# Kernel optimization log

Measured on AMD Instinct MI355X. Metric: run time of the kernel, lower is better.

The kernel has to match this reference:

```python
import jax, jax.numpy as jnp
import numpy as np

N_HEADS = 16
D_HEAD = 64
D_MODEL = 1024


def apply_rotary_emb(t, cos, sin):
    # t: (B, H, T, D), cos/sin: (T, D//2) -> half-split rotation
    d2 = t.shape[-1] // 2
    t1, t2 = t[..., :d2], t[..., d2:]
    cos = cos[None, None, :, :]
    sin = sin[None, None, :, :]
    return jnp.concatenate([t1 * cos - t2 * sin, t1 * sin + t2 * cos], axis=-1)


def setup_inputs() -> dict:
    key = jax.random.key(0)
    ks = jax.random.split(key, 8)
    B, T = 2, 2048
    x = jax.random.normal(ks[0], (B, T, D_MODEL), dtype=jnp.float32)
    # rotary cache built from standard inv-freq schedule
    inv_freq = 1.0 / (10000.0 ** (jnp.arange(0, D_HEAD, 2, dtype=jnp.float32) / D_HEAD))
    ang = jnp.arange(T, dtype=jnp.float32)[:, None] * inv_freq[None, :]  # (T, D/2)
    cos, sin = jnp.cos(ang), jnp.sin(ang)
    s = 1.0 / np.sqrt(D_MODEL)
    W_q = jax.random.normal(ks[1], (D_MODEL, N_HEADS * D_HEAD), dtype=jnp.float32) * s
    W_k = jax.random.normal(ks[2], (D_MODEL, N_HEADS * D_HEAD), dtype=jnp.float32) * s
    W_v = jax.random.normal(ks[3], (D_MODEL, N_HEADS * D_HEAD), dtype=jnp.float32) * s
    W_out = jax.random.normal(ks[4], (N_HEADS * D_HEAD, D_MODEL), dtype=jnp.float32) * s
    return {"x": x, "cos": cos, "sin": sin, "W_q": W_q, "W_k": W_k, "W_v": W_v, "W_out": W_out}


def reference(x, cos, sin, W_q, W_k, W_v, W_out):
    B, T, _ = x.shape
    def split_heads(t):
        return t.reshape(B, T, N_HEADS, D_HEAD).transpose(0, 2, 1, 3)  # (B,H,T,D)
    q = split_heads(x @ W_q)
    k = split_heads(x @ W_k)
    v = split_heads(x @ W_v)
    q = apply_rotary_emb(q, cos, sin)
    k = apply_rotary_emb(k, cos, sin)
    scores = jnp.einsum('bhqd,bhkd->bhqk', q, k) / np.sqrt(D_HEAD).astype(np.float32)
    causal = jnp.triu(jnp.ones((T, T), dtype=bool), k=1)
    scores = jnp.where(causal[None, None], -jnp.inf, scores)
    attn = jax.nn.softmax(scores, axis=-1)
    z = jnp.einsum('bhqk,bhkd->bhqd', attn, v)
    z = z.transpose(0, 2, 1, 3).reshape(B, T, N_HEADS * D_HEAD)
    return z @ W_out
```

## Files before the change

### kernel.cpp

```cpp
#include <hip/hip_runtime.h>

typedef __attribute__((ext_vector_type(4))) float f32x4;
typedef __attribute__((ext_vector_type(8))) short short8;
typedef __attribute__((ext_vector_type(8))) unsigned short u16x8;
typedef __attribute__((ext_vector_type(4))) unsigned short u16x4;
typedef __attribute__((ext_vector_type(2))) unsigned int u32x2;

#define D_MODEL 1024
#define NHEADS 16
#define T_SEQ 2048
#define M_TOT 4096

__device__ __forceinline__ unsigned short f2bf(float f) {
    union { float f; unsigned int u; } v; v.f = f;
    return (unsigned short)((v.u + 0x7fffu + ((v.u >> 16) & 1u)) >> 16);
}
__device__ __forceinline__ float bf2f(unsigned short b) {
    union { unsigned int u; float f; } v; v.u = ((unsigned int)b) << 16;
    return v.f;
}
__device__ __forceinline__ float bcf(unsigned int u) {
    union { unsigned int u; float f; } v; v.u = u; return v.f;
}
__device__ __forceinline__ unsigned int cvtpk_bf16(float lo, float hi) {
    unsigned int r;
    asm("v_cvt_pk_bf16_f32 %0, %1, %2" : "=v"(r) : "v"(lo), "v"(hi));
    return r;
}

#define GLD0(dst, addr) \
    asm volatile("global_load_dwordx4 %0, %1, off" : "=v"(dst) : "v"(addr) : "memory")
#define WAITV0() do { asm volatile("s_waitcnt vmcnt(0)" ::: "memory"); \
                      __builtin_amdgcn_sched_barrier(0); } while (0)
#define LBAR() do { asm volatile("s_waitcnt lgkmcnt(0)" ::: "memory"); \
                    __builtin_amdgcn_s_barrier(); \
                    __builtin_amdgcn_sched_barrier(0); } while (0)

__global__ __launch_bounds__(256) void convert_x_kernel(const float* __restrict__ X,
                                                        unsigned short* __restrict__ Xb) {
    const int i = (blockIdx.x * 256 + threadIdx.x) * 4;
    const float4 v = *(const float4*)(X + i);
    u16x4 r;
    r.x = f2bf(v.x); r.y = f2bf(v.y); r.z = f2bf(v.z); r.w = f2bf(v.w);
    *(u16x4*)(Xb + i) = r;
}

__global__ __launch_bounds__(256) void transpose_w_kernel(const float* __restrict__ W0,
                                                          const float* __restrict__ W1,
                                                          const float* __restrict__ W2,
                                                          const float* __restrict__ W3,
                                                          unsigned short* __restrict__ Wt0) {
    __shared__ float tile[64][65];
    const int z = blockIdx.z;
    const float* W = (z == 0) ? W0 : (z == 1) ? W1 : (z == 2) ? W2 : W3;
    unsigned short* Wt = Wt0 + (size_t)z * D_MODEL * D_MODEL;
    const int n0 = blockIdx.x * 64, k0 = blockIdx.y * 64;
    for (int i = threadIdx.x; i < 4096; i += 256) {
        const int r = i >> 6, c = i & 63;
        tile[r][c] = W[(size_t)(k0 + r) * D_MODEL + n0 + c];
    }
    __syncthreads();
    for (int i = threadIdx.x; i < 4096; i += 256) {
        const int r = i >> 6, c = i & 63;
        Wt[(size_t)(n0 + r) * D_MODEL + k0 + c] = f2bf(tile[c][r]);
    }
}

#define TN_G 128
#define BK_G 32
#define BKP_G 36

template<int MI, int OUTMODE>
__global__ __launch_bounds__(256) void gemm_kernel(
    const unsigned short* __restrict__ A,
    const unsigned short* __restrict__ Bt0,
    void* __restrict__ Cout0,
    const float* __restrict__ cosp,
    const float* __restrict__ sinp)
{
    constexpr int TMc = MI * 32;
    constexpr int NA = (TMc * 4) / 256;
    __shared__ unsigned short sA[TMc * BKP_G];
    __shared__ unsigned short sB[TN_G * BKP_G];

    const int tid = threadIdx.x;
    const int wid = tid >> 6;
    const int lane = tid & 63;
    const int quad = lane >> 4;
    const int l16 = lane & 15;
    const int wm = wid >> 1, wn = wid & 1;
    const int m0 = blockIdx.x * TMc, n0 = blockIdx.y * TN_G;
    const int z = blockIdx.z;
    const unsigned short* Bt = Bt0 + (size_t)z * D_MODEL * D_MODEL;

    f32x4 acc[MI][4] = {};

    for (int k0 = 0; k0 < D_MODEL; k0 += BK_G) {
        u16x8 av[NA], bv[2];
        #pragma unroll
        for (int i = 0; i < NA; ++i) {
            const int c = tid + i * 256, r = c >> 2, sg = (c & 3) * 8;
            av[i] = *(const u16x8*)(A + (size_t)(m0 + r) * D_MODEL + k0 + sg);
        }
        #pragma unroll
        for (int i = 0; i < 2; ++i) {
            const int c = tid + i * 256, r = c >> 2, sg = (c & 3) * 8;
            bv[i] = *(const u16x8*)(Bt + (size_t)(n0 + r) * D_MODEL + k0 + sg);
        }
        __syncthreads();
        #pragma unroll
        for (int i = 0; i < NA; ++i) {
            const int c = tid + i * 256, r = c >> 2, sg = (c & 3) * 8;
            *(u16x8*)&sA[r * BKP_G + sg] = av[i];
        }
        #pragma unroll
        for (int i = 0; i < 2; ++i) {
            const int c = tid + i * 256, r = c >> 2, sg = (c & 3) * 8;
            *(u16x8*)&sB[r * BKP_G + sg] = bv[i];
        }
        __syncthreads();

        short8 af[MI], bf[4];
        #pragma unroll
        for (int i = 0; i < MI; ++i)
            af[i] = *(const short8*)&sA[(wm * (MI * 16) + i * 16 + l16) * BKP_G + quad * 8];
        #pragma unroll
        for (int i = 0; i < 4; ++i)
            bf[i] = *(const short8*)&sB[(wn * 64 + i * 16 + l16) * BKP_G + quad * 8];
        #pragma unroll
        for (int mi = 0; mi < MI; ++mi)
            #pragma unroll
            for (int ni = 0; ni < 4; ++ni)
                acc[mi][ni] = __builtin_amdgcn_mfma_f32_16x16x32_bf16(af[mi], bf[ni], acc[mi][ni], 0, 0, 0);
    }

    if constexpr (OUTMODE == 0) {
        float* C = (float*)Cout0;
        #pragma unroll
        for (int mi = 0; mi < MI; ++mi) {
            const int mb = m0 + wm * (MI * 16) + mi * 16 + quad * 4;
            #pragma unroll
            for (int ni = 0; ni < 4; ++ni) {
                const int n = n0 + wn * 64 + ni * 16 + l16;
                #pragma unroll
                for (int r = 0; r < 4; ++r)
                    C[(size_t)(mb + r) * D_MODEL + n] = acc[mi][ni][r];
            }
        }
    } else {
        unsigned short* O = (unsigned short*)Cout0 + (size_t)z * M_TOT * D_MODEL;
        const int h = (n0 + wn * 64) >> 6;
        if (z == 2) {
            #pragma unroll
            for (int mi = 0; mi < MI; ++mi) {
                const int mb = m0 + wm * (MI * 16) + mi * 16 + quad * 4;
                const int b = mb >> 11, t = mb & (T_SEQ - 1);
                #pragma unroll
                for (int ni = 0; ni < 4; ++ni) {
                    const int d = ni * 16 + l16;
                    u16x4 pk;
                    #pragma unroll
                    for (int r = 0; r < 4; ++r) pk[r] = f2bf(acc[mi][ni][r]);
                    *(u16x4*)(O + ((size_t)(b * NHEADS + h) * 64 + d) * T_SEQ + t) = pk;
                }
            }
        } else {
            const float qs = (z == 0) ? 0.125f : 1.0f;
            #pragma unroll
            for (int mi = 0; mi < MI; ++mi) {
                #pragma unroll
                for (int r = 0; r < 4; ++r) {
                    const int m = m0 + wm * (MI * 16) + mi * 16 + quad * 4 + r;
                    const int b = m >> 11, t = m & (T_SEQ - 1);
                    const size_t rowoff = ((size_t)(b * NHEADS + h) * T_SEQ + t) * 64;
                    #pragma unroll
                    for (int ni = 0; ni < 2; ++ni) {
                        const int d = ni * 16 + l16;
                        const float c = cosp[t * 32 + d], s = sinp[t * 32 + d];
                        const float x1 = acc[mi][ni][r], x2 = acc[mi][ni + 2][r];
                        O[rowoff + d]      = f2bf((x1 * c - x2 * s) * qs);
                        O[rowoff + d + 32] = f2bf((x1 * s + x2 * c) * qs);
                    }
                }
            }
        }
    }
}

__global__ __launch_bounds__(256) void kmax_kernel(const unsigned short* __restrict__ Kg,
                                                   float* __restrict__ Kseg) {
    __shared__ float red[4];
    const int seg = blockIdx.x, bh = blockIdx.y;
    const unsigned short* Kp = Kg + ((size_t)bh * T_SEQ + seg * 256) * 64;
    const int row = threadIdx.x;
    const u16x8* rp = (const u16x8*)(Kp + (size_t)row * 64);
    float s = 0.f;
    #pragma unroll
    for (int c = 0; c < 8; ++c) {
        const u16x8 v = rp[c];
        #pragma unroll
        for (int e = 0; e < 8; ++e) { const float f = bf2f(v[e]); s += f * f; }
    }
    #pragma unroll
    for (int off = 32; off >= 1; off >>= 1) s = fmaxf(s, __shfl_xor(s, off));
    if ((threadIdx.x & 63) == 0) red[threadIdx.x >> 6] = s;
    __syncthreads();
    if (threadIdx.x == 0)
        Kseg[bh * 8 + seg] = __builtin_sqrtf(fmaxf(fmaxf(red[0], red[1]), fmaxf(red[2], red[3])));
}

#define LDPP 72
#define LOG2E 1.44269504f

struct AttnSmem {
    union {
        unsigned short kv[4][4096];
        float comb[4][64][34];
    } u;
    unsigned short P[8][16 * LDPP];
};

__global__ __launch_bounds__(512, 2) void attn_kernel(
    const unsigned short* __restrict__ Q,
    const unsigned short* __restrict__ Kg,
    const unsigned short* __restrict__ Vt,
    const float* __restrict__ Kseg,
    unsigned short* __restrict__ Z)
{
    __shared__ AttnSmem sm;

    const int tid = threadIdx.x;
    const int wid = tid >> 6;
    const int w4 = wid & 3;
    const int half = wid >> 2;
    const int lane = tid & 63;
    const int quad = lane >> 4;
    const int l16 = lane & 15;
    const int srow = tid >> 3;
    const int sslot = tid & 7;
    const int wslot = sslot ^ (srow & 7);
    const int sxK = (quad ^ (l16 & 7)) << 3;

    const int flat = blockIdx.x + 16 * blockIdx.y;
    const int xcd = flat & 7, idx = flat >> 3;
    const int bh = xcd * 4 + (idx & 3);
    const int x = idx >> 2;

    const int qA = x, qB = 31 - x;
    const int jend = 31 - x;

    const unsigned short* Qp = Q + (size_t)bh * T_SEQ * 64;
    const unsigned short* Kp = Kg + (size_t)bh * T_SEQ * 64;
    const unsigned short* Vp = Vt + (size_t)bh * 64 * T_SEQ;

    short8 aqA[2], aqB[2];
    {
        const unsigned short* qr = Qp + (size_t)(qA * 64 + w4 * 16 + l16) * 64 + quad * 8;
        aqA[0] = *(const short8*)(qr);
        aqA[1] = *(const short8*)(qr + 32);
        qr = Qp + (size_t)(qB * 64 + w4 * 16 + l16) * 64 + quad * 8;
        aqB[0] = *(const short8*)(qr);
        aqB[1] = *(const short8*)(qr + 32);
    }

    float kmx = 0.f;
    #pragma unroll
    for (int i = 0; i < 8; ++i) kmx = fmaxf(kmx, Kseg[bh * 8 + i]);

    float mQA, mQB;
    {
        float nqA = 0.f, nqB = 0.f;
        #pragma unroll
        for (int i = 0; i < 2; ++i)
            #pragma unroll
            for (int e = 0; e < 8; ++e) {
                const float fa = bf2f((unsigned short)aqA[i][e]);
                const float fb = bf2f((unsigned short)aqB[i][e]);
                nqA += fa * fa; nqB += fb * fb;
            }
        nqA += __shfl_xor(nqA, 16); nqA += __shfl_xor(nqA, 32);
        nqB += __shfl_xor(nqB, 16); nqB += __shfl_xor(nqB, 32);
        mQA = __builtin_sqrtf(nqA) * kmx * LOG2E;
        mQB = __builtin_sqrtf(nqB) * kmx * LOG2E;
    }

    auto tile_pack = [&](f32x4 (&s)[4], float mQ, float& lsum, bool msk,
                         unsigned short* Pw) {
        if (msk) {
            #pragma unroll
            for (int nt = 0; nt < 4; ++nt)
                #pragma unroll
                for (int r = 0; r < 4; ++r)
                    if (nt * 16 + quad * 4 + r > w4 * 16 + l16) s[nt][r] = -1e30f;
        }
        #pragma unroll
        for (int nt = 0; nt < 4; ++nt) {
            const float p0 = __builtin_exp2f(s[nt][0] * LOG2E - mQ);
            const float p1 = __builtin_exp2f(s[nt][1] * LOG2E - mQ);
            const float p2 = __builtin_exp2f(s[nt][2] * LOG2E - mQ);
            const float p3 = __builtin_exp2f(s[nt][3] * LOG2E - mQ);
            const unsigned int w0 = cvtpk_bf16(p0, p1);
            const unsigned int w1 = cvtpk_bf16(p2, p3);
            lsum += bcf(w0 << 16) + bcf(w0 & 0xffff0000u)
                  + bcf(w1 << 16) + bcf(w1 & 0xffff0000u);
            *(u32x2*)&Pw[(size_t)l16 * LDPP + nt * 16 + quad * 4] = (u32x2){w0, w1};
        }
    };

    f32x4 oA[4] = {}, oB[4] = {};
    float lA = 0.f, lB = 0.f;
    unsigned short* Pw = &sm.P[wid][0];
    const unsigned short* sKb = &sm.u.kv[half * 2][0];
    const unsigned short* sVb = &sm.u.kv[half * 2 + 1][0];

    short8 stg[4];
    auto ISSUE = [&](int t) {
        const int j0 = 2 * t, j1 = j0 + 1;
        GLD0(stg[0], Kp + (size_t)j0 * 4096 + tid * 8);
        GLD0(stg[1], Vp + (size_t)srow * 2048 + j0 * 64 + sslot * 8);
        GLD0(stg[2], Kp + (size_t)j1 * 4096 + tid * 8);
        GLD0(stg[3], Vp + (size_t)srow * 2048 + j1 * 64 + sslot * 8);
    };
    auto WRITE = [&] {
        const int dst = srow * 64 + (wslot << 3);
        *(short8*)&sm.u.kv[0][dst] = stg[0];
        *(short8*)&sm.u.kv[1][dst] = stg[1];
        *(short8*)&sm.u.kv[2][dst] = stg[2];
        *(short8*)&sm.u.kv[3][dst] = stg[3];
    };

    auto COMPUTE = [&](int j) {
        if (j > jend) return;
        const bool doA = (j <= x);
        f32x4 sA[4] = {}, sB[4] = {};
        #pragma unroll
        for (int nt = 0; nt < 4; ++nt) {
            const int rb = (nt * 16 + l16) * 64;
            const short8 k0 = *(const short8*)&sKb[rb + sxK];
            const short8 k1 = *(const short8*)&sKb[rb + (sxK ^ 32)];
            if (doA) {
                sA[nt] = __builtin_amdgcn_mfma_f32_16x16x32_bf16(k0, aqA[0], sA[nt], 0, 0, 0);
                sA[nt] = __builtin_amdgcn_mfma_f32_16x16x32_bf16(k1, aqA[1], sA[nt], 0, 0, 0);
            }
            sB[nt] = __builtin_amdgcn_mfma_f32_16x16x32_bf16(k0, aqB[0], sB[nt], 0, 0, 0);
            sB[nt] = __builtin_amdgcn_mfma_f32_16x16x32_bf16(k1, aqB[1], sB[nt], 0, 0, 0);
        }
        short8 pfA0 = {}, pfA1 = {};
        if (doA) {
            tile_pack(sA, mQA, lA, j == x, Pw);
            asm volatile("s_waitcnt lgkmcnt(0)" ::: "memory");
            pfA0 = *(const short8*)&Pw[(size_t)l16 * LDPP + quad * 8];
            pfA1 = *(const short8*)&Pw[(size_t)l16 * LDPP + 32 + quad * 8];
        }
        tile_pack(sB, mQB, lB, j == jend, Pw);
        asm volatile("s_waitcnt lgkmcnt(0)" ::: "memory");
        const short8 pfB0 = *(const short8*)&Pw[(size_t)l16 * LDPP + quad * 8];
        const short8 pfB1 = *(const short8*)&Pw[(size_t)l16 * LDPP + 32 + quad * 8];
        #pragma unroll
        for (int dt = 0; dt < 4; ++dt) {
            const int rb = (dt * 16 + l16) * 64;
            const short8 v0 = *(const short8*)&sVb[rb + sxK];
            const short8 v1 = *(const short8*)&sVb[rb + (sxK ^ 32)];
            if (doA) {
                oA[dt] = __builtin_amdgcn_mfma_f32_16x16x32_bf16(pfA0, v0, oA[dt], 0, 0, 0);
                oA[dt] = __builtin_amdgcn_mfma_f32_16x16x32_bf16(pfA1, v1, oA[dt], 0, 0, 0);
            }
            oB[dt] = __builtin_amdgcn_mfma_f32_16x16x32_bf16(pfB0, v0, oB[dt], 0, 0, 0);
            oB[dt] = __builtin_amdgcn_mfma_f32_16x16x32_bf16(pfB1, v1, oB[dt], 0, 0, 0);
        }
    };

    const int nr = (jend >> 1) + 1;
    ISSUE(0);
    WAITV0();
    WRITE();
    LBAR();
    for (int t = 0; t < nr; ++t) {
        const bool more = (t + 1 < nr);
        if (more) ISSUE(t + 1);
        COMPUTE(2 * t + half);
        LBAR();
        if (more) {
            WAITV0();
            WRITE();
            LBAR();
        }
    }

    lA += __shfl_xor(lA, 16); lA += __shfl_xor(lA, 32);
    lB += __shfl_xor(lB, 16); lB += __shfl_xor(lB, 32);

    __syncthreads();
    if (half) {
        float* cb = &sm.u.comb[w4][lane][0];
        #pragma unroll
        for (int dt = 0; dt < 4; ++dt)
            #pragma unroll
            for (int r = 0; r < 4; ++r) {
                cb[dt * 4 + r]      = oA[dt][r];
                cb[16 + dt * 4 + r] = oB[dt][r];
            }
        cb[32] = lA; cb[33] = lB;
    }
    __syncthreads();
    if (half) return;

    {
        const float* cb = &sm.u.comb[w4][lane][0];
        #pragma unroll
        for (int dt = 0; dt < 4; ++dt)
            #pragma unroll
            for (int r = 0; r < 4; ++r) {
                oA[dt][r] += cb[dt * 4 + r];
                oB[dt][r] += cb[16 + dt * 4 + r];
            }
        lA += cb[32]; lB += cb[33];
    }

    const float iA = 1.f / lA, iB = 1.f / lB;
    float irA[4], irB[4];
    #pragma unroll
    for (int r = 0; r < 4; ++r) {
        const int src = (lane & 48) | (quad * 4 + r);
        irA[r] = __shfl(iA, src);
        irB[r] = __shfl(iB, src);
    }

    const int h = bh & 15, b = bh >> 4;
    #pragma unroll
    for (int dt = 0; dt < 4; ++dt)
        #pragma unroll
        for (int r = 0; r < 4; ++r) {
            const int rowA = qA * 64 + w4 * 16 + quad * 4 + r;
            const int rowB = qB * 64 + w4 * 16 + quad * 4 + r;
            const int col = h * 64 + dt * 16 + l16;
            Z[((size_t)b * T_SEQ + rowA) * D_MODEL + col] = f2bf(oA[dt][r] * irA[r]);
            Z[((size_t)b * T_SEQ + rowB) * D_MODEL + col] = f2bf(oB[dt][r] * irB[r]);
        }
}

extern "C" void kernel_launch(void* const* d_in, const int* in_sizes, int n_in,
                              void* d_out, int out_size, void* d_ws, size_t ws_size,
                              hipStream_t stream) {
    const float* x    = (const float*)d_in[0];
    const float* cosp = (const float*)d_in[1];
    const float* sinp = (const float*)d_in[2];
    const float* Wq   = (const float*)d_in[3];
    const float* Wk   = (const float*)d_in[4];
    const float* Wv   = (const float*)d_in[5];
    const float* Wo   = (const float*)d_in[6];

    char* w = (char*)d_ws;
    unsigned short* xb  = (unsigned short*)w; w += (size_t)M_TOT * D_MODEL * 2;
    unsigned short* wt  = (unsigned short*)w; w += (size_t)4 * D_MODEL * D_MODEL * 2;
    unsigned short* Qb  = (unsigned short*)w; w += (size_t)M_TOT * D_MODEL * 2;
    unsigned short* Kb  = (unsigned short*)w; w += (size_t)M_TOT * D_MODEL * 2;
    unsigned short* Vtb = (unsigned short*)w; w += (size_t)M_TOT * D_MODEL * 2;
    unsigned short* Zb  = (unsigned short*)w; w += (size_t)M_TOT * D_MODEL * 2;
    float*          Ks  = (float*)w;          w += 32 * 8 * sizeof(float);

    convert_x_kernel<<<(M_TOT * D_MODEL) / 1024, 256, 0, stream>>>(x, xb);
    transpose_w_kernel<<<dim3(16, 16, 4), 256, 0, stream>>>(Wq, Wk, Wv, Wo, wt);

    gemm_kernel<4, 1><<<dim3(M_TOT / 128, D_MODEL / 128, 3), 256, 0, stream>>>(
        xb, wt, (void*)Qb, cosp, sinp);

    kmax_kernel<<<dim3(8, 32), 256, 0, stream>>>(Kb, Ks);

    attn_kernel<<<dim3(16, 32), 512, 0, stream>>>(Qb, Kb, Vtb, Ks, Zb);

    gemm_kernel<2, 0><<<dim3(M_TOT / 64, D_MODEL / 128, 1), 256, 0, stream>>>(
        Zb, wt + (size_t)3 * D_MODEL * D_MODEL, d_out, nullptr, nullptr);
}
```

Before: 220.2 us.

## Double-buffer K/V LDS tiles, swizzle P buffer, and raise priority around MFMA

The K/V shared-memory staging becomes double-buffered, so the next tile is written to the alternate buffer while the current one is consumed. This drops one of the two block barriers per iteration. The P scratch buffer loses its padded stride and uses an XOR swizzle instead, which shrinks LDS. The row sum is now taken from the fp32 probabilities rather than the bf16-rounded ones, and s_setprio is raised around the MFMA loops. The cost is doubled K/V LDS (32KB extra), which may reduce occupancy below the two blocks per CU the launch bounds ask for, plus a small numerical change in the normalizer.

```diff
diff --git a/kernel.cpp b/kernel.cpp
--- a/kernel.cpp
+++ b/kernel.cpp
@@ -18,9 +18,6 @@
 __device__ __forceinline__ float bf2f(unsigned short b) {
     union { unsigned int u; float f; } v; v.u = ((unsigned int)b) << 16;
     return v.f;
-}
-__device__ __forceinline__ float bcf(unsigned int u) {
-    union { unsigned int u; float f; } v; v.u = u; return v.f;
 }
 __device__ __forceinline__ unsigned int cvtpk_bf16(float lo, float hi) {
     unsigned int r;
@@ -209,15 +206,14 @@
         Kseg[bh * 8 + seg] = __builtin_sqrtf(fmaxf(fmaxf(red[0], red[1]), fmaxf(red[2], red[3])));
 }
 
-#define LDPP 72
 #define LOG2E 1.44269504f
 
 struct AttnSmem {
     union {
-        unsigned short kv[4][4096];
+        unsigned short kv[2][4][4096];
         float comb[4][64][34];
     } u;
-    unsigned short P[8][16 * LDPP];
+    unsigned short P[8][16 * 64];
 };
 
 __global__ __launch_bounds__(512, 2) void attn_kernel(
@@ -240,6 +236,7 @@
     const int sslot = tid & 7;
     const int wslot = sslot ^ (srow & 7);
     const int sxK = (quad ^ (l16 & 7)) << 3;
+    const int ph8 = (l16 & 7) << 3;
 
     const int flat = blockIdx.x + 16 * blockIdx.y;
     const int xcd = flat & 7, idx = flat >> 3;
@@ -299,19 +296,16 @@
             const float p1 = __builtin_exp2f(s[nt][1] * LOG2E - mQ);
             const float p2 = __builtin_exp2f(s[nt][2] * LOG2E - mQ);
             const float p3 = __builtin_exp2f(s[nt][3] * LOG2E - mQ);
+            lsum += (p0 + p1) + (p2 + p3);
             const unsigned int w0 = cvtpk_bf16(p0, p1);
             const unsigned int w1 = cvtpk_bf16(p2, p3);
-            lsum += bcf(w0 << 16) + bcf(w0 & 0xffff0000u)
-                  + bcf(w1 << 16) + bcf(w1 & 0xffff0000u);
-            *(u32x2*)&Pw[(size_t)l16 * LDPP + nt * 16 + quad * 4] = (u32x2){w0, w1};
+            *(u32x2*)&Pw[l16 * 64 + ((nt * 16 + quad * 4) ^ ph8)] = (u32x2){w0, w1};
         }
     };
 
     f32x4 oA[4] = {}, oB[4] = {};
     float lA = 0.f, lB = 0.f;
     unsigned short* Pw = &sm.P[wid][0];
-    const unsigned short* sKb = &sm.u.kv[half * 2][0];
-    const unsigned short* sVb = &sm.u.kv[half * 2 + 1][0];
 
     short8 stg[4];
     auto ISSUE = [&](int t) {
@@ -321,18 +315,21 @@
         GLD0(stg[2], Kp + (size_t)j1 * 4096 + tid * 8);
         GLD0(stg[3], Vp + (size_t)srow * 2048 + j1 * 64 + sslot * 8);
     };
-    auto WRITE = [&] {
+    auto WRITE = [&](int b) {
         const int dst = srow * 64 + (wslot << 3);
-        *(short8*)&sm.u.kv[0][dst] = stg[0];
-        *(short8*)&sm.u.kv[1][dst] = stg[1];
-        *(short8*)&sm.u.kv[2][dst] = stg[2];
-        *(short8*)&sm.u.kv[3][dst] = stg[3];
+        *(short8*)&sm.u.kv[b][0][dst] = stg[0];
+        *(short8*)&sm.u.kv[b][1][dst] = stg[1];
+        *(short8*)&sm.u.kv[b][2][dst] = stg[2];
+        *(short8*)&sm.u.kv[b][3][dst] = stg[3];
     };
 
-    auto COMPUTE = [&](int j) {
+    auto COMPUTE = [&](int j, int b) {
         if (j > jend) return;
         const bool doA = (j <= x);
+        const unsigned short* sKb = &sm.u.kv[b][half * 2][0];
+        const unsigned short* sVb = &sm.u.kv[b][half * 2 + 1][0];
         f32x4 sA[4] = {}, sB[4] = {};
+        __builtin_amdgcn_s_setprio(1);
         #pragma unroll
         for (int nt = 0; nt < 4; ++nt) {
             const int rb = (nt * 16 + l16) * 64;
@@ -345,17 +342,19 @@
             sB[nt] = __builtin_amdgcn_mfma_f32_16x16x32_bf16(k0, aqB[0], sB[nt], 0, 0, 0);
             sB[nt] = __builtin_amdgcn_mfma_f32_16x16x32_bf16(k1, aqB[1], sB[nt], 0, 0, 0);
         }
+        __builtin_amdgcn_s_setprio(0);
         short8 pfA0 = {}, pfA1 = {};
         if (doA) {
             tile_pack(sA, mQA, lA, j == x, Pw);
             asm volatile("s_waitcnt lgkmcnt(0)" ::: "memory");
-            pfA0 = *(const short8*)&Pw[(size_t)l16 * LDPP + quad * 8];
-            pfA1 = *(const short8*)&Pw[(size_t)l16 * LDPP + 32 + quad * 8];
+            pfA0 = *(const short8*)&Pw[l16 * 64 + ((quad * 8) ^ ph8)];
+            pfA1 = *(const short8*)&Pw[l16 * 64 + ((32 + quad * 8) ^ ph8)];
         }
         tile_pack(sB, mQB, lB, j == jend, Pw);
         asm volatile("s_waitcnt lgkmcnt(0)" ::: "memory");
-        const short8 pfB0 = *(const short8*)&Pw[(size_t)l16 * LDPP + quad * 8];
-        const short8 pfB1 = *(const short8*)&Pw[(size_t)l16 * LDPP + 32 + quad * 8];
+        const short8 pfB0 = *(const short8*)&Pw[l16 * 64 + ((quad * 8) ^ ph8)];
+        const short8 pfB1 = *(const short8*)&Pw[l16 * 64 + ((32 + quad * 8) ^ ph8)];
+        __builtin_amdgcn_s_setprio(1);
         #pragma unroll
         for (int dt = 0; dt < 4; ++dt) {
             const int rb = (dt * 16 + l16) * 64;
@@ -368,23 +367,23 @@
             oB[dt] = __builtin_amdgcn_mfma_f32_16x16x32_bf16(pfB0, v0, oB[dt], 0, 0, 0);
             oB[dt] = __builtin_amdgcn_mfma_f32_16x16x32_bf16(pfB1, v1, oB[dt], 0, 0, 0);
         }
+        __builtin_amdgcn_s_setprio(0);
     };
 
     const int nr = (jend >> 1) + 1;
     ISSUE(0);
     WAITV0();
-    WRITE();
+    WRITE(0);
     LBAR();
     for (int t = 0; t < nr; ++t) {
         const bool more = (t + 1 < nr);
         if (more) ISSUE(t + 1);
-        COMPUTE(2 * t + half);
-        LBAR();
+        COMPUTE(2 * t + half, t & 1);
         if (more) {
             WAITV0();
-            WRITE();
-            LBAR();
-        }
+            WRITE((t + 1) & 1);
+        }
+        LBAR();
     }
 
     lA += __shfl_xor(lA, 16); lA += __shfl_xor(lA, 32);
```

Measured after the change: 216.1 us. About the same (-1.8%).
